# Optimization experiments

Measured on AMD Instinct MI355X. Metric: run time of the kernel, lower is better.

Reference implementation:

```python
import jax, jax.numpy as jnp
import numpy as np

B, T, D, H = 4, 2048, 384, 6
HD = D // H  # 64
HALF = HD // 2


def setup_inputs() -> dict:
    key = jax.random.key(0)
    k0, k1, k2 = jax.random.split(key, 3)
    x = jax.random.normal(k0, (B, T, D), jnp.float32)
    attn_bias = jnp.zeros((1, 1, T, T), jnp.float32)  # additive SDPA bias
    # standard RoPE tables: [T, HD/2]
    inv_freq = 1.0 / (10000.0 ** (np.arange(HALF, dtype=np.float32) / HALF))
    ang = np.arange(T, dtype=np.float32)[:, None] * inv_freq[None, :]
    cos = jnp.asarray(np.cos(ang), jnp.float32)
    sin = jnp.asarray(np.sin(ang), jnp.float32)
    w_qkv = jax.random.normal(k1, (D, 3 * D), jnp.float32) * (D ** -0.5)
    w_proj = jax.random.normal(k2, (D, D), jnp.float32) * (D ** -0.5)
    return {"x": x, "attn_bias": attn_bias, "cos": cos, "sin": sin,
            "w_qkv": w_qkv, "w_proj": w_proj}


def _apply_rope(x, cos, sin):
    # x: [b, h, t, hd]; cos/sin: [t, hd/2] -> rotate-half RoPE
    half = x.shape[-1] // 2
    x1, x2 = x[..., :half], x[..., half:]
    c = cos[None, None, :, :]
    s = sin[None, None, :, :]
    return jnp.concatenate([x1 * c - x2 * s, x2 * c + x1 * s], axis=-1)


def reference(x, attn_bias, cos, sin, w_qkv, w_proj):
    b, t, _ = x.shape
    qkv = (x @ w_qkv).reshape(b, t, 3, H, HD)  # fused QKV projection
    q = jnp.transpose(qkv[:, :, 0], (0, 2, 1, 3))  # [b,h,t,hd]
    k = jnp.transpose(qkv[:, :, 1], (0, 2, 1, 3))
    v = jnp.transpose(qkv[:, :, 2], (0, 2, 1, 3))
    q = _apply_rope(q, cos, sin)
    k = _apply_rope(k, cos, sin)
    scale = 1.0 / jnp.sqrt(jnp.asarray(HD, x.dtype))
    scores = jnp.einsum("bhqd,bhkd->bhqk", q, k) * scale + attn_bias
    attn = jax.nn.softmax(scores, axis=-1)
    out = jnp.einsum("bhqk,bhkd->bhqd", attn, v)
    out = jnp.transpose(out, (0, 2, 1, 3)).reshape(b, t, H * HD)
    return out @ w_proj
```

## Files before the change

kernel.cpp:

```cpp
#include <hip/hip_runtime.h>
#include <hip/hip_bf16.h>

#define BB   4
#define TT   2048
#define DDIM 384
#define HH   6
#define HD   64
#define BT   (BB*TT)
#define QKVC (3*DDIM)

typedef __attribute__((ext_vector_type(4))) short short4v;
typedef __attribute__((ext_vector_type(8))) short short8v;
typedef __attribute__((ext_vector_type(4))) float float4v;
typedef unsigned short u16;

static __device__ __forceinline__ u16 f2bu(float f) {
    __hip_bfloat16 h = __float2bfloat16(f);
    return __builtin_bit_cast(u16, h);
}

static __device__ __forceinline__ short8v ld_frag(const u16* p) {
    short4v a = *(const short4v*)p;
    short4v b = *(const short4v*)(p + 4);
    return __builtin_shufflevector(a, b, 0, 1, 2, 3, 4, 5, 6, 7);
}

static __device__ __forceinline__ void st8(u16* p, uint4 v) {
    *(uint2*)p       = make_uint2(v.x, v.y);
    *(uint2*)(p + 4) = make_uint2(v.z, v.w);
}

#define MFMA16(a, b, c) __builtin_amdgcn_mfma_f32_16x16x32_bf16((a), (b), (c), 0, 0, 0)

#if __has_builtin(__builtin_amdgcn_mfma_f32_16x16x16_bf16)
#define MFMAK16(a, b, c) __builtin_amdgcn_mfma_f32_16x16x16_bf16((a), (b), (c), 0, 0, 0)
#elif __has_builtin(__builtin_amdgcn_mfma_f32_16x16x16bf16_1k)
#define MFMAK16(a, b, c) __builtin_amdgcn_mfma_f32_16x16x16bf16_1k((a), (b), (c), 0, 0, 0)
#else
#define MFMAK16(a, b, c) __builtin_amdgcn_mfma_f32_16x16x16bf16_1k((a), (b), (c), 0, 0, 0)
#endif

__global__ __launch_bounds__(256) void prep_kernel(
    const float* __restrict__ wqkv, const float* __restrict__ wproj,
    const float* __restrict__ x,
    u16* __restrict__ wqkvT, u16* __restrict__ wprojT, u16* __restrict__ xb)
{
    const int bid = blockIdx.x;
    const int t = threadIdx.x;
    if (bid >= 144) {
        size_t base = (size_t)(bid - 144) * 4096 + (size_t)t * 16;
        const float* gp = x + base;
        __align__(16) u16 tmp[16];
        #pragma unroll
        for (int u = 0; u < 4; ++u) {
            float4 v = *(const float4*)(gp + 4 * u);
            tmp[4 * u + 0] = f2bu(v.x); tmp[4 * u + 1] = f2bu(v.y);
            tmp[4 * u + 2] = f2bu(v.z); tmp[4 * u + 3] = f2bu(v.w);
        }
        *(uint4*)(xb + base)     = *(const uint4*)tmp;
        *(uint4*)(xb + base + 8) = *(const uint4*)(tmp + 8);
        return;
    }
    const float* in; u16* out; int K, C, c0, k0;
    if (bid < 108) { in = wqkv;  out = wqkvT;  K = DDIM; C = QKVC;
                     c0 = (bid % 18) * 64; k0 = (bid / 18) * 64; }
    else           { int b2 = bid - 108; in = wproj; out = wprojT; K = DDIM; C = DDIM;
                     c0 = (b2 % 6) * 64; k0 = (b2 / 6) * 64; }
    __shared__ float tr[64][65];
    {
        int kr = t >> 2, cb = (t & 3) * 16;
        const float* gp = in + (size_t)(k0 + kr) * C + c0 + cb;
        #pragma unroll
        for (int u = 0; u < 4; ++u) {
            float4 v = *(const float4*)(gp + 4 * u);
            tr[cb + 4 * u + 0][kr] = v.x;
            tr[cb + 4 * u + 1][kr] = v.y;
            tr[cb + 4 * u + 2][kr] = v.z;
            tr[cb + 4 * u + 3][kr] = v.w;
        }
    }
    __syncthreads();
    {
        int c = t >> 2, kb = (t & 3) * 16;
        __align__(16) u16 tmp[16];
        #pragma unroll
        for (int u = 0; u < 16; ++u) tmp[u] = f2bu(tr[c][kb + u]);
        u16* op = out + (size_t)(c0 + c) * K + k0 + kb;
        *(uint4*)op       = *(const uint4*)tmp;
        *(uint4*)(op + 8) = *(const uint4*)(tmp + 8);
    }
}

__global__ __launch_bounds__(256) void qkv_rope_kernel(
    const u16* __restrict__ xb, const u16* __restrict__ wt,
    const float* __restrict__ cs, const float* __restrict__ sn,
    u16* __restrict__ qb, u16* __restrict__ kb, u16* __restrict__ vtb)
{
    __shared__ __align__(16) u16 xs[2][64][68];
    __shared__ __align__(16) u16 ws[2][64][68];
    const int t = threadIdx.x;
    const int wv = t >> 6, lane = t & 63, quad = lane >> 4, lo = lane & 15;
    const int r0 = blockIdx.y * 64;
    const int c0 = blockIdx.x * 64;
    const int sr = t >> 3, sd = (t & 7) * 8;

    st8(&xs[0][sr][sd],      *(const uint4*)(xb + (size_t)(r0 + sr) * DDIM + sd));
    st8(&xs[0][sr + 32][sd], *(const uint4*)(xb + (size_t)(r0 + sr + 32) * DDIM + sd));
    st8(&ws[0][sr][sd],      *(const uint4*)(wt + (size_t)(c0 + sr) * DDIM + sd));
    st8(&ws[0][sr + 32][sd], *(const uint4*)(wt + (size_t)(c0 + sr + 32) * DDIM + sd));
    __syncthreads();

    float4v acc[4] = {};
    for (int kk = 0; kk < 6; ++kk) {
        const int cur = kk & 1, nxt = cur ^ 1;
        const int kkn = (kk < 5 ? kk + 1 : 5) * 64;
        uint4 xp0 = *(const uint4*)(xb + (size_t)(r0 + sr) * DDIM + kkn + sd);
        uint4 xp1 = *(const uint4*)(xb + (size_t)(r0 + sr + 32) * DDIM + kkn + sd);
        uint4 wp0 = *(const uint4*)(wt + (size_t)(c0 + sr) * DDIM + kkn + sd);
        uint4 wp1 = *(const uint4*)(wt + (size_t)(c0 + sr + 32) * DDIM + kkn + sd);

        #pragma unroll
        for (int kf = 0; kf < 2; ++kf) {
            short8v a = ld_frag(&xs[cur][16 * wv + lo][kf * 32 + quad * 8]);
            #pragma unroll
            for (int nt = 0; nt < 4; ++nt) {
                short8v b = ld_frag(&ws[cur][nt * 16 + lo][kf * 32 + quad * 8]);
                acc[nt] = MFMA16(a, b, acc[nt]);
            }
        }
        st8(&xs[nxt][sr][sd], xp0);
        st8(&xs[nxt][sr + 32][sd], xp1);
        st8(&ws[nxt][sr][sd], wp0);
        st8(&ws[nxt][sr + 32][sd], wp1);
        __syncthreads();
    }

    const int sec = blockIdx.x / 6;
    const int h   = blockIdx.x % 6;
    const int rbase = r0 + 16 * wv + 4 * quad;
    const int bidx  = r0 >> 11;
    const int tbase = rbase & (TT - 1);

    if (sec == 2) {
        #pragma unroll
        for (int nt = 0; nt < 4; ++nt) {
            int d = nt * 16 + lo;
            unsigned a0 = f2bu(acc[nt][0]) | ((unsigned)f2bu(acc[nt][1]) << 16);
            unsigned a1 = f2bu(acc[nt][2]) | ((unsigned)f2bu(acc[nt][3]) << 16);
            u16* gp = vtb + ((size_t)(bidx * HH + h) * HD + d) * TT + tbase;
            *(uint2*)gp = make_uint2(a0, a1);
        }
    } else {
        u16* dst = (sec == 0) ? qb : kb;
        #pragma unroll
        for (int np = 0; np < 2; ++np) {
            #pragma unroll
            for (int r = 0; r < 4; ++r) {
                int tpos = tbase + r;
                int ci = np * 16 + lo;
                float cv = cs[tpos * 32 + ci];
                float sv = sn[tpos * 32 + ci];
                float x1 = acc[np][r], x2 = acc[np + 2][r];
                u16* gp = dst + ((size_t)(bidx * HH + h) * TT + tpos) * HD;
                gp[ci]      = f2bu(x1 * cv - x2 * sv);
                gp[ci + 32] = f2bu(x2 * cv + x1 * sv);
            }
        }
    }
}

__global__ __launch_bounds__(256, 3) void attn_kernel(
    const u16* __restrict__ qb, const u16* __restrict__ kb, const u16* __restrict__ vtb,
    const float* __restrict__ bias, u16* __restrict__ ob)
{
    __shared__ __align__(16) u16 ks[2][64][68];
    __shared__ __align__(16) u16 vt[2][64][68];

    const int t = threadIdx.x;
    const int wv = t >> 6, lane = t & 63, quad = lane >> 4, lo = lane & 15;
    const int bh = blockIdx.y;
    const int b = bh / HH, h = bh % HH;
    const int q0 = blockIdx.x * 64;
    const int qrow = q0 + 16 * wv + lo;

    const u16* qbase = qb + ((size_t)bh * TT + qrow) * HD + quad * 8;
    short8v aq0 = __builtin_bit_cast(short8v, *(const uint4*)qbase);
    short8v aq1 = __builtin_bit_cast(short8v, *(const uint4*)(qbase + 32));

    const int sr = t >> 3, sd = (t & 7) * 8;
    const u16* kbbase = kb + (size_t)bh * TT * HD;
    const u16* vtbase = vtb + (size_t)bh * HD * TT;
    const float* brow = bias + (size_t)qrow * TT + 4 * quad;

    st8(&ks[0][sr][sd],      *(const uint4*)(kbbase + (size_t)sr * HD + sd));
    st8(&ks[0][sr + 32][sd], *(const uint4*)(kbbase + (size_t)(sr + 32) * HD + sd));
    st8(&vt[0][sr][sd],      *(const uint4*)(vtbase + (size_t)sr * TT + sd));
    st8(&vt[0][sr + 32][sd], *(const uint4*)(vtbase + (size_t)(sr + 32) * TT + sd));
    float4 bcur[4];
    #pragma unroll
    for (int nt = 0; nt < 4; ++nt) bcur[nt] = *(const float4*)(brow + nt * 16);
    __syncthreads();

    float4v oacc[4] = {};
    float lacc[4] = {0.f, 0.f, 0.f, 0.f};

    for (int kt = 0; kt < TT / 64; ++kt) {
        const int cur = kt & 1, nxt = cur ^ 1;
        const int kn = (kt < 31 ? kt + 1 : 31) * 64;

        uint4 kp0 = *(const uint4*)(kbbase + (size_t)(kn + sr) * HD + sd);
        uint4 kp1 = *(const uint4*)(kbbase + (size_t)(kn + sr + 32) * HD + sd);
        uint4 vp0 = *(const uint4*)(vtbase + (size_t)sr * TT + kn + sd);
        uint4 vp1 = *(const uint4*)(vtbase + (size_t)(sr + 32) * TT + kn + sd);
        float4 bnxt[4];
        #pragma unroll
        for (int nt = 0; nt < 4; ++nt) bnxt[nt] = *(const float4*)(brow + kn + nt * 16);

        float4v s[4] = {};
        #pragma unroll
        for (int kf = 0; kf < 2; ++kf) {
            #pragma unroll
            for (int nt = 0; nt < 4; ++nt) {
                short8v kfr = ld_frag(&ks[cur][nt * 16 + lo][kf * 32 + quad * 8]);
                s[nt] = MFMA16(kfr, (kf ? aq1 : aq0), s[nt]);
            }
        }

        short4v pa[4];
        #pragma unroll
        for (int nt = 0; nt < 4; ++nt) {
            float p0 = __expf(fmaf(s[nt][0], 0.125f, bcur[nt].x));
            float p1 = __expf(fmaf(s[nt][1], 0.125f, bcur[nt].y));
            float p2 = __expf(fmaf(s[nt][2], 0.125f, bcur[nt].z));
            float p3 = __expf(fmaf(s[nt][3], 0.125f, bcur[nt].w));
            lacc[nt] += (p0 + p1) + (p2 + p3);
            short4v pv = { (short)f2bu(p0), (short)f2bu(p1),
                           (short)f2bu(p2), (short)f2bu(p3) };
            pa[nt] = pv;
        }

        #pragma unroll
        for (int dt = 0; dt < 4; ++dt) {
            #pragma unroll
            for (int nt = 0; nt < 4; ++nt) {
                short4v bv = *(const short4v*)&vt[cur][dt * 16 + lo][nt * 16 + 4 * quad];
                oacc[dt] = MFMAK16(pa[nt], bv, oacc[dt]);
            }
        }

        st8(&ks[nxt][sr][sd], kp0);
        st8(&ks[nxt][sr + 32][sd], kp1);
        st8(&vt[nxt][sr][sd], vp0);
        st8(&vt[nxt][sr + 32][sd], vp1);
        #pragma unroll
        for (int nt = 0; nt < 4; ++nt) bcur[nt] = bnxt[nt];
        __syncthreads();
    }

    float l = (lacc[0] + lacc[1]) + (lacc[2] + lacc[3]);
    l += __shfl_xor(l, 16);
    l += __shfl_xor(l, 32);
    #pragma unroll
    for (int r = 0; r < 4; ++r) {
        float lr = __shfl(l, 4 * quad + r);
        float inv = 1.f / lr;
        u16* gp = ob + ((size_t)b * TT + q0 + 16 * wv + 4 * quad + r) * DDIM + h * HD + lo;
        #pragma unroll
        for (int dt = 0; dt < 4; ++dt)
            gp[dt * 16] = f2bu(oacc[dt][r] * inv);
    }
}

__global__ __launch_bounds__(256) void proj_kernel(
    const u16* __restrict__ o, const u16* __restrict__ wt, float* __restrict__ out)
{
    __shared__ __align__(16) u16 os[2][64][68];
    __shared__ __align__(16) u16 ws[2][64][68];
    const int t = threadIdx.x;
    const int wv = t >> 6, lane = t & 63, quad = lane >> 4, lo = lane & 15;
    const int r0 = blockIdx.y * 64, c0 = blockIdx.x * 64;
    const int sr = t >> 3, sd = (t & 7) * 8;

    st8(&os[0][sr][sd],      *(const uint4*)(o + (size_t)(r0 + sr) * DDIM + sd));
    st8(&os[0][sr + 32][sd], *(const uint4*)(o + (size_t)(r0 + sr + 32) * DDIM + sd));
    st8(&ws[0][sr][sd],      *(const uint4*)(wt + (size_t)(c0 + sr) * DDIM + sd));
    st8(&ws[0][sr + 32][sd], *(const uint4*)(wt + (size_t)(c0 + sr + 32) * DDIM + sd));
    __syncthreads();

    float4v acc[4] = {};
    for (int kk = 0; kk < 6; ++kk) {
        const int cur = kk & 1, nxt = cur ^ 1;
        const int kkn = (kk < 5 ? kk + 1 : 5) * 64;
        uint4 op0 = *(const uint4*)(o + (size_t)(r0 + sr) * DDIM + kkn + sd);
        uint4 op1 = *(const uint4*)(o + (size_t)(r0 + sr + 32) * DDIM + kkn + sd);
        uint4 wp0 = *(const uint4*)(wt + (size_t)(c0 + sr) * DDIM + kkn + sd);
        uint4 wp1 = *(const uint4*)(wt + (size_t)(c0 + sr + 32) * DDIM + kkn + sd);

        #pragma unroll
        for (int kf = 0; kf < 2; ++kf) {
            short8v a = ld_frag(&os[cur][16 * wv + lo][kf * 32 + quad * 8]);
            #pragma unroll
            for (int nt = 0; nt < 4; ++nt) {
                short8v bfr = ld_frag(&ws[cur][nt * 16 + lo][kf * 32 + quad * 8]);
                acc[nt] = MFMA16(a, bfr, acc[nt]);
            }
        }
        st8(&os[nxt][sr][sd], op0);
        st8(&os[nxt][sr + 32][sd], op1);
        st8(&ws[nxt][sr][sd], wp0);
        st8(&ws[nxt][sr + 32][sd], wp1);
        __syncthreads();
    }
    #pragma unroll
    for (int r = 0; r < 4; ++r) {
        float* gp = out + (size_t)(r0 + 16 * wv + 4 * quad + r) * DDIM + c0;
        #pragma unroll
        for (int nt = 0; nt < 4; ++nt)
            gp[nt * 16 + lo] = acc[nt][r];
    }
}

extern "C" void kernel_launch(void* const* d_in, const int* in_sizes, int n_in,
                              void* d_out, int out_size, void* d_ws, size_t ws_size,
                              hipStream_t stream) {
    const float* x     = (const float*)d_in[0];
    const float* bias  = (const float*)d_in[1];
    const float* cs    = (const float*)d_in[2];
    const float* sn    = (const float*)d_in[3];
    const float* wqkv  = (const float*)d_in[4];
    const float* wproj = (const float*)d_in[5];
    float* out = (float*)d_out;

    u16* wqkvT  = (u16*)d_ws;
    u16* wprojT = wqkvT + (size_t)QKVC * DDIM;
    u16* qb     = wprojT + (size_t)DDIM * DDIM;
    u16* kb     = qb + (size_t)BB * HH * TT * HD;
    u16* vtb    = kb + (size_t)BB * HH * TT * HD;
    u16* ob     = vtb + (size_t)BB * HH * TT * HD;
    u16* xb     = ob + (size_t)BT * DDIM;

    prep_kernel<<<dim3(144 + BT * DDIM / 4096), 256, 0, stream>>>(
        wqkv, wproj, x, wqkvT, wprojT, xb);
    qkv_rope_kernel<<<dim3(QKVC / 64, BT / 64), 256, 0, stream>>>(
        xb, wqkvT, cs, sn, qb, kb, vtb);
    attn_kernel<<<dim3(TT / 64, BB * HH), 256, 0, stream>>>(qb, kb, vtb, bias, ob);
    proj_kernel<<<dim3(DDIM / 64, BT / 64), 256, 0, stream>>>(ob, wprojT, out);
}
```

Before: 191.3 us.

## Split keys across waves in attention, drop LDS staging, and store bias as bf16

The attention kernel is restructured so that each wave covers all 64 query rows of the block but only a 16-key slice of every 64-key tile. K, V and bias fragments are now loaded straight from global memory into registers with one-iteration prefetch, replacing the double-buffered LDS tiles and the per-iteration barrier. The four waves' partial outputs and row sums are combined through LDS at the end. The additive bias is converted to bf16 in the prep kernel to halve its large repeated reads, and the grid order is swapped so blocks sharing a query tile run together and can reuse the bias in cache. RoPE outputs are packed into 32-bit stores with an interleaved head-dim order that Q and K share, so QK dot products are unchanged. The costs are bf16 rounding of the bias, more registers per wave, and an extra prep pass over the bias.

```diff
diff --git a/kernel.cpp b/kernel.cpp
--- a/kernel.cpp
+++ b/kernel.cpp
@@ -18,6 +18,10 @@
     __hip_bfloat16 h = __float2bfloat16(f);
     return __builtin_bit_cast(u16, h);
 }
+static __device__ __forceinline__ float bu2f(u16 v) {
+    unsigned u = (unsigned)v << 16;
+    return __builtin_bit_cast(float, u);
+}
 
 static __device__ __forceinline__ short8v ld_frag(const u16* p) {
     short4v a = *(const short4v*)p;
@@ -34,22 +38,24 @@
 
 #if __has_builtin(__builtin_amdgcn_mfma_f32_16x16x16_bf16)
 #define MFMAK16(a, b, c) __builtin_amdgcn_mfma_f32_16x16x16_bf16((a), (b), (c), 0, 0, 0)
-#elif __has_builtin(__builtin_amdgcn_mfma_f32_16x16x16bf16_1k)
-#define MFMAK16(a, b, c) __builtin_amdgcn_mfma_f32_16x16x16bf16_1k((a), (b), (c), 0, 0, 0)
 #else
 #define MFMAK16(a, b, c) __builtin_amdgcn_mfma_f32_16x16x16bf16_1k((a), (b), (c), 0, 0, 0)
 #endif
 
 __global__ __launch_bounds__(256) void prep_kernel(
     const float* __restrict__ wqkv, const float* __restrict__ wproj,
-    const float* __restrict__ x,
-    u16* __restrict__ wqkvT, u16* __restrict__ wprojT, u16* __restrict__ xb)
+    const float* __restrict__ x, const float* __restrict__ bias,
+    u16* __restrict__ wqkvT, u16* __restrict__ wprojT,
+    u16* __restrict__ xb, u16* __restrict__ biasb)
 {
     const int bid = blockIdx.x;
     const int t = threadIdx.x;
     if (bid >= 144) {
-        size_t base = (size_t)(bid - 144) * 4096 + (size_t)t * 16;
-        const float* gp = x + base;
+        const float* src; u16* dst; size_t base;
+        if (bid < 912) { src = x;    dst = xb;    base = (size_t)(bid - 144) * 4096; }
+        else           { src = bias; dst = biasb; base = (size_t)(bid - 912) * 4096; }
+        base += (size_t)t * 16;
+        const float* gp = src + base;
         __align__(16) u16 tmp[16];
         #pragma unroll
         for (int u = 0; u < 4; ++u) {
@@ -57,8 +63,8 @@
             tmp[4 * u + 0] = f2bu(v.x); tmp[4 * u + 1] = f2bu(v.y);
             tmp[4 * u + 2] = f2bu(v.z); tmp[4 * u + 3] = f2bu(v.w);
         }
-        *(uint4*)(xb + base)     = *(const uint4*)tmp;
-        *(uint4*)(xb + base + 8) = *(const uint4*)(tmp + 8);
+        *(uint4*)(dst + base)     = *(const uint4*)tmp;
+        *(uint4*)(dst + base + 8) = *(const uint4*)(tmp + 8);
         return;
     }
     const float* in; u16* out; int K, C, c0, k0;
@@ -161,9 +167,10 @@
                 float cv = cs[tpos * 32 + ci];
                 float sv = sn[tpos * 32 + ci];
                 float x1 = acc[np][r], x2 = acc[np + 2][r];
-                u16* gp = dst + ((size_t)(bidx * HH + h) * TT + tpos) * HD;
-                gp[ci]      = f2bu(x1 * cv - x2 * sv);
-                gp[ci + 32] = f2bu(x2 * cv + x1 * sv);
+                unsigned pk = f2bu(x1 * cv - x2 * sv) |
+                              ((unsigned)f2bu(x2 * cv + x1 * sv) << 16);
+                unsigned* gp = (unsigned*)(dst + ((size_t)(bidx * HH + h) * TT + tpos) * HD);
+                gp[ci] = pk;
             }
         }
     }
@@ -171,103 +178,133 @@
 
 __global__ __launch_bounds__(256, 3) void attn_kernel(
     const u16* __restrict__ qb, const u16* __restrict__ kb, const u16* __restrict__ vtb,
-    const float* __restrict__ bias, u16* __restrict__ ob)
+    const u16* __restrict__ biasb, u16* __restrict__ ob)
 {
-    __shared__ __align__(16) u16 ks[2][64][68];
-    __shared__ __align__(16) u16 vt[2][64][68];
+    __shared__ __align__(16) float obuf[4][16][68];
+    __shared__ float lred[4][64];
 
     const int t = threadIdx.x;
     const int wv = t >> 6, lane = t & 63, quad = lane >> 4, lo = lane & 15;
-    const int bh = blockIdx.y;
+    const int bh = blockIdx.x;
     const int b = bh / HH, h = bh % HH;
-    const int q0 = blockIdx.x * 64;
-    const int qrow = q0 + 16 * wv + lo;
-
-    const u16* qbase = qb + ((size_t)bh * TT + qrow) * HD + quad * 8;
-    short8v aq0 = __builtin_bit_cast(short8v, *(const uint4*)qbase);
-    short8v aq1 = __builtin_bit_cast(short8v, *(const uint4*)(qbase + 32));
-
-    const int sr = t >> 3, sd = (t & 7) * 8;
-    const u16* kbbase = kb + (size_t)bh * TT * HD;
-    const u16* vtbase = vtb + (size_t)bh * HD * TT;
-    const float* brow = bias + (size_t)qrow * TT + 4 * quad;
-
-    st8(&ks[0][sr][sd],      *(const uint4*)(kbbase + (size_t)sr * HD + sd));
-    st8(&ks[0][sr + 32][sd], *(const uint4*)(kbbase + (size_t)(sr + 32) * HD + sd));
-    st8(&vt[0][sr][sd],      *(const uint4*)(vtbase + (size_t)sr * TT + sd));
-    st8(&vt[0][sr + 32][sd], *(const uint4*)(vtbase + (size_t)(sr + 32) * TT + sd));
-    float4 bcur[4];
-    #pragma unroll
-    for (int nt = 0; nt < 4; ++nt) bcur[nt] = *(const float4*)(brow + nt * 16);
+    const int q0 = blockIdx.y * 64;
+
+    short8v aq[4][2];
+    #pragma unroll
+    for (int s = 0; s < 4; ++s) {
+        const u16* qp = qb + ((size_t)bh * TT + q0 + 16 * s + lo) * HD + quad * 8;
+        aq[s][0] = __builtin_bit_cast(short8v, *(const uint4*)qp);
+        aq[s][1] = __builtin_bit_cast(short8v, *(const uint4*)(qp + 32));
+    }
+
+    const u16* kp = kb + ((size_t)bh * TT + 16 * wv + lo) * HD + quad * 8;
+    const u16* vp = vtb + ((size_t)bh * HD + lo) * TT + 16 * wv + 4 * quad;
+    const u16* bp = biasb + (size_t)(q0 + lo) * TT + 16 * wv + 4 * quad;
+
+    uint4 pk0 = *(const uint4*)kp;
+    uint4 pk1 = *(const uint4*)(kp + 32);
+    uint2 pv[4], pb[4];
+    #pragma unroll
+    for (int dt = 0; dt < 4; ++dt) pv[dt] = *(const uint2*)(vp + (size_t)dt * 16 * TT);
+    #pragma unroll
+    for (int s = 0; s < 4; ++s)  pb[s] = *(const uint2*)(bp + (size_t)s * 16 * TT);
+
+    float4v oacc[4][4] = {};
+    float lacc[4] = {0.f, 0.f, 0.f, 0.f};
+
+    for (int kt = 0; kt < TT / 64; ++kt) {
+        short8v ka0 = __builtin_bit_cast(short8v, pk0);
+        short8v ka1 = __builtin_bit_cast(short8v, pk1);
+        short4v vb[4];
+        uint2 bcur[4];
+        #pragma unroll
+        for (int dt = 0; dt < 4; ++dt) vb[dt] = __builtin_bit_cast(short4v, pv[dt]);
+        #pragma unroll
+        for (int s = 0; s < 4; ++s) bcur[s] = pb[s];
+
+        const int adv = (kt < TT / 64 - 1) ? 64 : 0;
+        kp += (size_t)adv * HD;  vp += adv;  bp += adv;
+        pk0 = *(const uint4*)kp;
+        pk1 = *(const uint4*)(kp + 32);
+        #pragma unroll
+        for (int dt = 0; dt < 4; ++dt) pv[dt] = *(const uint2*)(vp + (size_t)dt * 16 * TT);
+        #pragma unroll
+        for (int s = 0; s < 4; ++s)  pb[s] = *(const uint2*)(bp + (size_t)s * 16 * TT);
+
+        float4v sv[4];
+        #pragma unroll
+        for (int s = 0; s < 4; ++s) {
+            float4v z = {};
+            sv[s] = MFMA16(ka0, aq[s][0], z);
+            sv[s] = MFMA16(ka1, aq[s][1], sv[s]);
+        }
+
+        short4v pa[4];
+        #pragma unroll
+        for (int s = 0; s < 4; ++s) {
+            float b0 = bu2f((u16)(bcur[s].x & 0xffff));
+            float b1 = bu2f((u16)(bcur[s].x >> 16));
+            float b2 = bu2f((u16)(bcur[s].y & 0xffff));
+            float b3 = bu2f((u16)(bcur[s].y >> 16));
+            float p0 = __expf(fmaf(sv[s][0], 0.125f, b0));
+            float p1 = __expf(fmaf(sv[s][1], 0.125f, b1));
+            float p2 = __expf(fmaf(sv[s][2], 0.125f, b2));
+            float p3 = __expf(fmaf(sv[s][3], 0.125f, b3));
+            lacc[s] += (p0 + p1) + (p2 + p3);
+            short4v pvv = { (short)f2bu(p0), (short)f2bu(p1),
+                            (short)f2bu(p2), (short)f2bu(p3) };
+            pa[s] = pvv;
+        }
+
+        #pragma unroll
+        for (int s = 0; s < 4; ++s)
+            #pragma unroll
+            for (int dt = 0; dt < 4; ++dt)
+                oacc[s][dt] = MFMAK16(pa[s], vb[dt], oacc[s][dt]);
+    }
+
+    #pragma unroll
+    for (int s = 0; s < 4; ++s) {
+        lacc[s] += __shfl_xor(lacc[s], 16);
+        lacc[s] += __shfl_xor(lacc[s], 32);
+    }
+    if (quad == 0) {
+        #pragma unroll
+        for (int s = 0; s < 4; ++s) lred[wv][s * 16 + lo] = lacc[s];
+    }
+    #pragma unroll
+    for (int dt = 0; dt < 4; ++dt)
+        #pragma unroll
+        for (int r = 0; r < 4; ++r)
+            obuf[wv][4 * quad + r][16 * dt + lo] = oacc[0][dt][r];
     __syncthreads();
 
-    float4v oacc[4] = {};
-    float lacc[4] = {0.f, 0.f, 0.f, 0.f};
-
-    for (int kt = 0; kt < TT / 64; ++kt) {
-        const int cur = kt & 1, nxt = cur ^ 1;
-        const int kn = (kt < 31 ? kt + 1 : 31) * 64;
-
-        uint4 kp0 = *(const uint4*)(kbbase + (size_t)(kn + sr) * HD + sd);
-        uint4 kp1 = *(const uint4*)(kbbase + (size_t)(kn + sr + 32) * HD + sd);
-        uint4 vp0 = *(const uint4*)(vtbase + (size_t)sr * TT + kn + sd);
-        uint4 vp1 = *(const uint4*)(vtbase + (size_t)(sr + 32) * TT + kn + sd);
-        float4 bnxt[4];
-        #pragma unroll
-        for (int nt = 0; nt < 4; ++nt) bnxt[nt] = *(const float4*)(brow + kn + nt * 16);
-
-        float4v s[4] = {};
-        #pragma unroll
-        for (int kf = 0; kf < 2; ++kf) {
-            #pragma unroll
-            for (int nt = 0; nt < 4; ++nt) {
-                short8v kfr = ld_frag(&ks[cur][nt * 16 + lo][kf * 32 + quad * 8]);
-                s[nt] = MFMA16(kfr, (kf ? aq1 : aq0), s[nt]);
-            }
-        }
-
-        short4v pa[4];
-        #pragma unroll
-        for (int nt = 0; nt < 4; ++nt) {
-            float p0 = __expf(fmaf(s[nt][0], 0.125f, bcur[nt].x));
-            float p1 = __expf(fmaf(s[nt][1], 0.125f, bcur[nt].y));
-            float p2 = __expf(fmaf(s[nt][2], 0.125f, bcur[nt].z));
-            float p3 = __expf(fmaf(s[nt][3], 0.125f, bcur[nt].w));
-            lacc[nt] += (p0 + p1) + (p2 + p3);
-            short4v pv = { (short)f2bu(p0), (short)f2bu(p1),
-                           (short)f2bu(p2), (short)f2bu(p3) };
-            pa[nt] = pv;
-        }
-
-        #pragma unroll
-        for (int dt = 0; dt < 4; ++dt) {
-            #pragma unroll
-            for (int nt = 0; nt < 4; ++nt) {
-                short4v bv = *(const short4v*)&vt[cur][dt * 16 + lo][nt * 16 + 4 * quad];
-                oacc[dt] = MFMAK16(pa[nt], bv, oacc[dt]);
-            }
-        }
-
-        st8(&ks[nxt][sr][sd], kp0);
-        st8(&ks[nxt][sr + 32][sd], kp1);
-        st8(&vt[nxt][sr][sd], vp0);
-        st8(&vt[nxt][sr + 32][sd], vp1);
-        #pragma unroll
-        for (int nt = 0; nt < 4; ++nt) bcur[nt] = bnxt[nt];
+    const int i = t >> 4, j4 = (t & 15) * 4;
+    #pragma unroll
+    for (int s = 0; s < 4; ++s) {
+        float4 s0 = *(const float4*)&obuf[0][i][j4];
+        float4 s1 = *(const float4*)&obuf[1][i][j4];
+        float4 s2 = *(const float4*)&obuf[2][i][j4];
+        float4 s3 = *(const float4*)&obuf[3][i][j4];
+        float inv = 1.f / (lred[0][s * 16 + i] + lred[1][s * 16 + i] +
+                           lred[2][s * 16 + i] + lred[3][s * 16 + i]);
+        float o0 = (s0.x + s1.x + s2.x + s3.x) * inv;
+        float o1 = (s0.y + s1.y + s2.y + s3.y) * inv;
+        float o2 = (s0.z + s1.z + s2.z + s3.z) * inv;
+        float o3 = (s0.w + s1.w + s2.w + s3.w) * inv;
+        unsigned a0 = f2bu(o0) | ((unsigned)f2bu(o1) << 16);
+        unsigned a1 = f2bu(o2) | ((unsigned)f2bu(o3) << 16);
+        u16* gp = ob + ((size_t)b * TT + q0 + 16 * s + i) * DDIM + h * HD + j4;
+        *(uint2*)gp = make_uint2(a0, a1);
         __syncthreads();
-    }
-
-    float l = (lacc[0] + lacc[1]) + (lacc[2] + lacc[3]);
-    l += __shfl_xor(l, 16);
-    l += __shfl_xor(l, 32);
-    #pragma unroll
-    for (int r = 0; r < 4; ++r) {
-        float lr = __shfl(l, 4 * quad + r);
-        float inv = 1.f / lr;
-        u16* gp = ob + ((size_t)b * TT + q0 + 16 * wv + 4 * quad + r) * DDIM + h * HD + lo;
-        #pragma unroll
-        for (int dt = 0; dt < 4; ++dt)
-            gp[dt * 16] = f2bu(oacc[dt][r] * inv);
+        if (s < 3) {
+            #pragma unroll
+            for (int dt = 0; dt < 4; ++dt)
+                #pragma unroll
+                for (int r = 0; r < 4; ++r)
+                    obuf[wv][4 * quad + r][16 * dt + lo] = oacc[s + 1][dt][r];
+            __syncthreads();
+        }
     }
 }
 
@@ -338,11 +375,13 @@
     u16* vtb    = kb + (size_t)BB * HH * TT * HD;
     u16* ob     = vtb + (size_t)BB * HH * TT * HD;
     u16* xb     = ob + (size_t)BT * DDIM;
-
-    prep_kernel<<<dim3(144 + BT * DDIM / 4096), 256, 0, stream>>>(
-        wqkv, wproj, x, wqkvT, wprojT, xb);
+    u16* biasb  = xb + (size_t)BT * DDIM;
+
+    prep_kernel<<<dim3(144 + 768 + 1024), 256, 0, stream>>>(
+        wqkv, wproj, x, bias, wqkvT, wprojT, xb, biasb);
     qkv_rope_kernel<<<dim3(QKVC / 64, BT / 64), 256, 0, stream>>>(
         xb, wqkvT, cs, sn, qb, kb, vtb);
-    attn_kernel<<<dim3(TT / 64, BB * HH), 256, 0, stream>>>(qb, kb, vtb, bias, ob);
+    attn_kernel<<<dim3(BB * HH, TT / 64), 256, 0, stream>>>(
+        qb, kb, vtb, biasb, ob);
     proj_kernel<<<dim3(DDIM / 64, BT / 64), 256, 0, stream>>>(ob, wprojT, out);
 }
```

Result: slower. 227.8 us (+19.1%).
